# Optimization experiments

Hardware: AMD Instinct MI355X
Metric: run time of the kernel (lower is better)

Reference implementation:

```python
import jax, jax.numpy as jnp
import numpy as np

EPS = 1e-5
NEIGHBOR_K = 3
NEG_SLOPE = 0.2

def _conv(x, w):
    # x: [N,C,H,W], w: [O,I,3,3], stride 1, SAME padding
    return jax.lax.conv_general_dilated(
        x, w, window_strides=(1, 1), padding='SAME',
        dimension_numbers=('NCHW', 'OIHW', 'NCHW'))

def _bn(x, gamma, beta):
    # BatchNorm2d in training mode: batch statistics over (N,H,W), biased var
    m = x.mean(axis=(0, 2, 3), keepdims=True)
    v = x.var(axis=(0, 2, 3), keepdims=True)
    xn = (x - m) * jax.lax.rsqrt(v + EPS)
    return xn * gamma.reshape(1, -1, 1, 1) + beta.reshape(1, -1, 1, 1)

def _lrelu(x):
    return jnp.where(x >= 0, x, NEG_SLOPE * x)

def _maxpool2(x):
    return jax.lax.reduce_window(x, -jnp.inf, jax.lax.max,
                                 (1, 1, 2, 2), (1, 1, 2, 2), 'VALID')

def _features(x, w1, g1, b1, w2, g2, b2, w3, g3, b3, w4, g4, b4):
    x = _maxpool2(_lrelu(_bn(_conv(x, w1), g1, b1)))
    x = _maxpool2(_lrelu(_bn(_conv(x, w2), g2, b2)))
    x = _lrelu(_bn(_conv(x, w3), g3, b3))
    x = _lrelu(_bn(_conv(x, w4), g4, b4))
    return x  # [N, 64, 21, 21]

def setup_inputs() -> dict:
    key = jax.random.key(0)
    ks = jax.random.split(key, 8)
    inp = {
        'input1': jax.random.normal(ks[0], (32, 3, 84, 84), jnp.float32),
        'input2': jax.random.normal(ks[1], (5, 5, 3, 84, 84), jnp.float32),
        'w1': jax.random.normal(ks[2], (64, 3, 3, 3), jnp.float32) * 0.1,
        'g1': jax.random.uniform(ks[3], (64,), jnp.float32, 0.5, 1.5),
        'b1': jnp.zeros((64,), jnp.float32),
        'w2': jax.random.normal(ks[4], (64, 64, 3, 3), jnp.float32) * 0.1,
        'g2': jax.random.uniform(ks[5], (64,), jnp.float32, 0.5, 1.5),
        'b2': jnp.zeros((64,), jnp.float32),
        'w3': jax.random.normal(ks[6], (64, 64, 3, 3), jnp.float32) * 0.1,
        'g3': jax.random.uniform(ks[7], (64,), jnp.float32, 0.5, 1.5),
        'b3': jnp.zeros((64,), jnp.float32),
        'w4': jax.random.normal(jax.random.fold_in(key, 100), (64, 64, 3, 3), jnp.float32) * 0.1,
        'g4': jax.random.uniform(jax.random.fold_in(key, 101), (64,), jnp.float32, 0.5, 1.5),
        'b4': jnp.zeros((64,), jnp.float32),
    }
    return inp

def reference(input1, input2, w1, g1, b1, w2, g2, b2, w3, g3, b3, w4, g4, b4):
    params = (w1, g1, b1, w2, g2, b2, w3, g3, b3, w4, g4, b4)
    # Query features: [B, C, h, w]
    q = _features(input1, *params)
    B, C, h, w = q.shape
    hw = h * w
    Q = q.reshape(B, C, hw).transpose(0, 2, 1)            # [B, hw, C]
    qn = jnp.linalg.norm(Q, axis=2, keepdims=True)        # [B, hw, 1]
    # Support features, BN stats per class-batch (matches per-class forward)
    s = jax.vmap(lambda x: _features(x, *params))(input2) # [nc, shot, C, h, w]
    nc, shot = s.shape[0], s.shape[1]
    S = s.transpose(0, 2, 1, 3, 4).reshape(nc, C, shot * hw)  # [nc, C, M]
    sn = jnp.linalg.norm(S, axis=1, keepdims=True)            # [nc, 1, M]
    # Cosine similarities: [B, nc, hw, M]
    sims = jnp.einsum('bqc,ncm->bnqm', Q, S)
    sims = sims / (qn[:, None, :, :] * sn[None, :, :, :])
    topv = jax.lax.top_k(sims, NEIGHBOR_K)[0]              # [B, nc, hw, k]
    return topv.sum(axis=(2, 3))                           # [B, nc]
```

## Files before the change

kernel.cpp:

```cpp
#include <hip/hip_runtime.h>
#include <hip/hip_bf16.h>
#include <stdint.h>

#define NQ 32
#define NCLS 5
#define SHOT 5
#define NIMG 57
#define P1 7056
#define P2 1764
#define P3 441
#define PX 3528
#define MM (SHOT*P3)
#define EPSB 1e-5f
#define SLOPE 0.2f
#define NEGINF -3.4e38f
#define NREP 32
#define MSPAN 1152
#define MRNG 2
#define QBLK 128
#define NQB 4
#define QG 2
#define SLS 72
#define BNPIX 32

typedef __attribute__((ext_vector_type(8))) short short8;
typedef __attribute__((ext_vector_type(4))) float f32x4;

__device__ __forceinline__ unsigned short bf16bits(float v)
{
    __hip_bfloat16 h = __float2bfloat16(v);
    return *reinterpret_cast<unsigned short*>(&h);
}
__device__ __forceinline__ float bits2f(unsigned short u)
{
    unsigned int x = ((unsigned int)u) << 16;
    return *reinterpret_cast<float*>(&x);
}

__global__ void pack_all_k(const float* __restrict__ w1, const float* __restrict__ w2,
                           const float* __restrict__ w3, const float* __restrict__ w4,
                           unsigned short* __restrict__ wpk1, unsigned short* __restrict__ wpk2,
                           unsigned short* __restrict__ wpk3, unsigned short* __restrict__ wpk4,
                           float* __restrict__ sums)
{
    int i = blockIdx.x * 256 + threadIdx.x;
    if (i < 4 * 6 * 64 * 2 * NREP) sums[i] = 0.f;
    if (i < 3 * 36864) {
        int set = i / 36864, ii = i - set * 36864;
        const float* w = (set == 0) ? w2 : (set == 1) ? w3 : w4;
        unsigned short* wpk = (set == 0) ? wpk2 : (set == 1) ? wpk3 : wpk4;
        int j = ii & 7, lane = (ii >> 3) & 63, chunk = ii >> 9;
        int nt = chunk & 3, half = (chunk >> 2) & 1, t = chunk >> 3;
        int co = nt * 16 + (lane & 15);
        int ci = half * 32 + (lane >> 4) * 8 + j;
        wpk[ii] = bf16bits(w[co * 576 + ci * 9 + t]);
    } else {
        int ii = i - 3 * 36864;
        if (ii >= 4096) return;
        int j = ii & 7, lane = (ii >> 3) & 63, c8 = ii >> 9;
        int nt = c8 & 3, f = c8 >> 2;
        int co = nt * 16 + (lane & 15), q = lane >> 4;
        int k = q * 8 + j;
        float val = 0.f;
        if (f == 0) {
            int t = k >> 2, ci = k & 3;
            if (ci < 3) val = w1[co * 27 + ci * 9 + t];
        } else if (k < 4) {
            int ci = k & 3;
            if (ci < 3) val = w1[co * 27 + ci * 9 + 8];
        }
        wpk1[ii] = bf16bits(val);
    }
}

__global__ __launch_bounds__(256) void conv1m_k(const float* __restrict__ in1,
                                                const float* __restrict__ in2,
                                                const unsigned short* __restrict__ wpk1,
                                                __hip_bfloat16* __restrict__ xpool,
                                                float* __restrict__ sums)
{
    constexpr int S = 84, P = P1, MBLK = 256, NB = 28, SPAN = MBLK + 2 * S + 2;
    __shared__ __align__(16) unsigned short ls4[SPAN * 4];
    __shared__ float qs[4][64], qs2[4][64];
    int img = blockIdx.x / NB;
    int p0 = (blockIdx.x % NB) * MBLK;
    int tid = threadIdx.x, lane = tid & 63, wv = tid >> 6;
    int col = lane & 15, quad = lane >> 4;
    const float* in = (img < NQ) ? in1 + (size_t)img * 3 * P1
                                 : in2 + (size_t)(img - NQ) * 3 * P1;
    for (int u = tid; u < SPAN; u += 256) {
        int p = p0 - S - 1 + u;
        union { unsigned short us[4]; uint2 u2; } o;
        o.u2 = (uint2){0u, 0u};
        if (p >= 0 && p < P) {
            o.us[0] = bf16bits(in[p]);
            o.us[1] = bf16bits(in[P1 + p]);
            o.us[2] = bf16bits(in[2 * P1 + p]);
        }
        *(uint2*)(ls4 + u * 4) = o.u2;
    }
    const short8* wb = (const short8*)wpk1;
    short8 b0[4], b1[4];
    #pragma unroll
    for (int nt = 0; nt < 4; ++nt) {
        b0[nt] = wb[(size_t)(nt * 64 + lane)];
        b1[nt] = wb[(size_t)((4 + nt) * 64 + lane)];
    }
    int t0 = 2 * quad, t1 = t0 + 1;
    int d0 = (t0 / 3 - 1) * S + (t0 % 3 - 1);
    int d1 = (t1 / 3 - 1) * S + (t1 % 3 - 1);
    const int d8 = S + 1;
    int tx0 = t0 % 3, tx1 = t1 % 3;
    __syncthreads();
    f32x4 acc[4][4];
    #pragma unroll
    for (int mt = 0; mt < 4; ++mt)
        #pragma unroll
        for (int nt = 0; nt < 4; ++nt) acc[mt][nt] = (f32x4){0.f, 0.f, 0.f, 0.f};
    #pragma unroll
    for (int mt = 0; mt < 4; ++mt) {
        int pl = wv * 64 + mt * 16 + col;
        int xm = (p0 + pl) % S;
        int base = pl + S + 1;
        uint2 h0 = *(const uint2*)(ls4 + (base + d0) * 4);
        uint2 h1 = *(const uint2*)(ls4 + (base + d1) * 4);
        uint2 h8 = *(const uint2*)(ls4 + (base + d8) * 4);
        bool ok0 = (tx0 == 0) ? (xm >= 1) : ((tx0 == 2) ? (xm <= S - 2) : true);
        bool ok1 = (tx1 == 0) ? (xm >= 1) : ((tx1 == 2) ? (xm <= S - 2) : true);
        bool ok8 = (quad == 0) && (xm <= S - 2);
        if (!ok0) h0 = (uint2){0u, 0u};
        if (!ok1) h1 = (uint2){0u, 0u};
        if (!ok8) h8 = (uint2){0u, 0u};
        union { uint4 u; short8 s; } ca, cb;
        ca.u = (uint4){h0.x, h0.y, h1.x, h1.y};
        cb.u = (uint4){h8.x, h8.y, 0u, 0u};
        #pragma unroll
        for (int nt = 0; nt < 4; ++nt) {
            acc[mt][nt] = __builtin_amdgcn_mfma_f32_16x16x32_bf16(ca.s, b0[nt], acc[mt][nt], 0, 0, 0);
            acc[mt][nt] = __builtin_amdgcn_mfma_f32_16x16x32_bf16(cb.s, b1[nt], acc[mt][nt], 0, 0, 0);
        }
    }
    float s[4] = {0.f, 0.f, 0.f, 0.f}, s2[4] = {0.f, 0.f, 0.f, 0.f};
    __hip_bfloat16* ob = xpool + (size_t)img * PX * 64;
    #pragma unroll
    for (int mt = 0; mt < 4; ++mt) {
        int tb = p0 + wv * 64 + mt * 16 + quad * 4;
        #pragma unroll
        for (int reg = 0; reg < 4; ++reg) {
            int pr = tb + reg;
            if (pr < P) {
                #pragma unroll
                for (int nt = 0; nt < 4; ++nt) {
                    float v = acc[mt][nt][reg];
                    s[nt] += v;
                    s2[nt] = fmaf(v, v, s2[nt]);
                }
            }
        }
        #pragma unroll
        for (int pr2 = 0; pr2 < 2; ++pr2) {
            int m0 = tb + pr2 * 2;
            if (m0 < P) {
                #pragma unroll
                for (int nt = 0; nt < 4; ++nt) {
                    float v = fmaxf(acc[mt][nt][pr2 * 2], acc[mt][nt][pr2 * 2 + 1]);
                    ob[(size_t)(m0 >> 1) * 64 + nt * 16 + col] = __float2bfloat16(v);
                }
            }
        }
    }
    #pragma unroll
    for (int d = 16; d < 64; d <<= 1)
        #pragma unroll
        for (int nt = 0; nt < 4; ++nt) {
            s[nt] += __shfl_xor(s[nt], d, 64);
            s2[nt] += __shfl_xor(s2[nt], d, 64);
        }
    if (quad == 0) {
        #pragma unroll
        for (int nt = 0; nt < 4; ++nt) {
            qs[wv][nt * 16 + col] = s[nt];
            qs2[wv][nt * 16 + col] = s2[nt];
        }
    }
    __syncthreads();
    if (wv == 0) {
        int g = (img < NQ) ? 0 : 1 + (img - NQ) / SHOT;
        int rep = blockIdx.x & (NREP - 1);
        float ts = qs[0][lane] + qs[1][lane] + qs[2][lane] + qs[3][lane];
        float ts2 = qs2[0][lane] + qs2[1][lane] + qs2[2][lane] + qs2[3][lane];
        float* base = sums + ((size_t)(g * 64 + lane) * 2) * NREP + rep;
        atomicAdd(base, ts);
        atomicAdd(base + NREP, ts2);
    }
}

template <int PREVP>
__device__ __forceinline__ void bn_fold(const float* __restrict__ sums_prev,
                                        const float* __restrict__ gamma,
                                        const float* __restrict__ beta,
                                        int g, int tid, float* msl)
{
    if (tid < 64) {
        const float* ps = sums_prev + (size_t)(g * 64 + tid) * 2 * NREP;
        float s = 0.f, s2 = 0.f;
        #pragma unroll
        for (int r = 0; r < NREP; ++r) { s += ps[r]; s2 += ps[NREP + r]; }
        float cnt = (float)((g == 0 ? NQ : SHOT) * PREVP);
        float mean = s / cnt;
        float var = s2 / cnt - mean * mean;
        float a = rsqrtf(var + EPSB) * gamma[tid];
        msl[tid * 2] = a;
        msl[tid * 2 + 1] = fmaf(-mean, a, beta[tid]);
    }
}

template <int S, int MBLK, int MODE, bool POOLX, int PREVP>
__global__ __launch_bounds__(256) void conv64m_k(const unsigned short* __restrict__ inv,
                                                 const unsigned short* __restrict__ wpk,
                                                 __hip_bfloat16* __restrict__ out,
                                                 float* __restrict__ sums,
                                                 const float* __restrict__ sums_prev,
                                                 const float* __restrict__ gamma,
                                                 const float* __restrict__ beta)
{
    constexpr int P = S * S;
    constexpr int MT = MBLK / 64;
    constexpr int NB = (P + MBLK - 1) / MBLK;
    constexpr int SPAN = MBLK + 2 * S + 2;
    __shared__ __align__(16) unsigned short ls[SPAN * 72];
    __shared__ float qs[4][64], qs2[4][64];
    __shared__ float msl[128];
    int img = blockIdx.x / NB;
    int p0 = (blockIdx.x % NB) * MBLK;
    int tid = threadIdx.x;
    int lane = tid & 63, wv = tid >> 6;
    int col = lane & 15, quad = lane >> 4;
    int g = (img < NQ) ? 0 : 1 + (img - NQ) / SHOT;
    bn_fold<PREVP>(sums_prev, gamma, beta, g, tid, msl);
    __syncthreads();
    {
        int part = tid & 7;
        float ba[8], bb[8];
        #pragma unroll
        for (int j = 0; j < 8; ++j) {
            ba[j] = msl[(part * 8 + j) * 2];
            bb[j] = msl[(part * 8 + j) * 2 + 1];
        }
        if constexpr (MODE == 1) {
            const unsigned short* ib = inv + (size_t)img * P * 64;
            for (int u = tid; u < SPAN * 8; u += 256) {
                int pix = u >> 3;
                int p = p0 - S - 1 + pix;
                union { unsigned short us[8]; short8 s8; } o;
                #pragma unroll
                for (int j = 0; j < 8; ++j) o.us[j] = 0;
                if (p >= 0 && p < P) {
                    union { short8 s8; unsigned short us[8]; } x;
                    x.s8 = *(const short8*)(ib + (size_t)p * 64 + part * 8);
                    #pragma unroll
                    for (int j = 0; j < 8; ++j) {
                        float v = fmaf(bits2f(x.us[j]), ba[j], bb[j]);
                        v = fmaxf(v, SLOPE * v);
                        o.us[j] = bf16bits(v);
                    }
                }
                *(short8*)(ls + pix * 72 + part * 8) = o.s8;
            }
        } else {
            const unsigned short* ib2 = inv + (size_t)img * (2 * (size_t)P) * 64;
            for (int u = tid; u < SPAN * 8; u += 256) {
                int pix = u >> 3;
                int p = p0 - S - 1 + pix;
                union { unsigned short us[8]; short8 s8; } o;
                #pragma unroll
                for (int j = 0; j < 8; ++j) o.us[j] = 0;
                if (p >= 0 && p < P) {
                    int y = p / S, x = p - y * S;
                    const unsigned short* src = ib2 + ((size_t)(2 * y) * S + x) * 64 + part * 8;
                    union { short8 s8; unsigned short us[8]; } x0, x1;
                    x0.s8 = *(const short8*)src;
                    x1.s8 = *(const short8*)(src + (size_t)S * 64);
                    #pragma unroll
                    for (int j = 0; j < 8; ++j) {
                        float v = fmaxf(bits2f(x0.us[j]), bits2f(x1.us[j]));
                        v = fmaf(v, ba[j], bb[j]);
                        v = fmaxf(v, SLOPE * v);
                        o.us[j] = bf16bits(v);
                    }
                }
                *(short8*)(ls + pix * 72 + part * 8) = o.s8;
            }
        }
    }
    __syncthreads();
    f32x4 acc[MT][4];
    #pragma unroll
    for (int mt = 0; mt < MT; ++mt)
        #pragma unroll
        for (int nt = 0; nt < 4; ++nt) acc[mt][nt] = (f32x4){0.f, 0.f, 0.f, 0.f};
    bool mok0[MT], mok2[MT];
    #pragma unroll
    for (int mt = 0; mt < MT; ++mt) {
        int xm = (p0 + wv * (MT * 16) + mt * 16 + col) % S;
        mok0[mt] = xm >= 1;
        mok2[mt] = xm <= S - 2;
    }
    const short8* wb = (const short8*)wpk;
    #pragma unroll
    for (int ky = 0; ky < 3; ++ky) {
        #pragma unroll
        for (int kx = 0; kx < 3; ++kx) {
            int t = ky * 3 + kx;
            int d = (ky - 1) * S + (kx - 1);
            #pragma unroll
            for (int half = 0; half < 2; ++half) {
                short8 b[4];
                #pragma unroll
                for (int nt = 0; nt < 4; ++nt)
                    b[nt] = wb[((t * 2 + half) * 4 + nt) * 64 + lane];
                #pragma unroll
                for (int mt = 0; mt < MT; ++mt) {
                    int idx = wv * (MT * 16) + mt * 16 + col + S + 1 + d;
                    short8 a = *(const short8*)(ls + idx * 72 + half * 32 + quad * 8);
                    bool ok = (kx == 0) ? mok0[mt] : (kx == 2) ? mok2[mt] : true;
                    if (!ok) a = (short8){0, 0, 0, 0, 0, 0, 0, 0};
                    #pragma unroll
                    for (int nt = 0; nt < 4; ++nt)
                        acc[mt][nt] = __builtin_amdgcn_mfma_f32_16x16x32_bf16(a, b[nt], acc[mt][nt], 0, 0, 0);
                }
            }
        }
    }
    float s[4] = {0.f, 0.f, 0.f, 0.f}, s2[4] = {0.f, 0.f, 0.f, 0.f};
    __hip_bfloat16* ob = out + (size_t)img * (POOLX ? P / 2 : P) * 64;
    #pragma unroll
    for (int mt = 0; mt < MT; ++mt) {
        int tb = p0 + wv * (MT * 16) + mt * 16 + quad * 4;
        #pragma unroll
        for (int reg = 0; reg < 4; ++reg) {
            int pr = tb + reg;
            if (pr < P) {
                #pragma unroll
                for (int nt = 0; nt < 4; ++nt) {
                    float v = acc[mt][nt][reg];
                    s[nt] += v;
                    s2[nt] = fmaf(v, v, s2[nt]);
                }
            }
        }
        if constexpr (POOLX) {
            #pragma unroll
            for (int pr2 = 0; pr2 < 2; ++pr2) {
                int m0 = tb + pr2 * 2;
                if (m0 < P) {
                    #pragma unroll
                    for (int nt = 0; nt < 4; ++nt) {
                        float v = fmaxf(acc[mt][nt][pr2 * 2], acc[mt][nt][pr2 * 2 + 1]);
                        ob[(size_t)(m0 >> 1) * 64 + nt * 16 + col] = __float2bfloat16(v);
                    }
                }
            }
        } else {
            #pragma unroll
            for (int reg = 0; reg < 4; ++reg) {
                int pr = tb + reg;
                if (pr < P) {
                    #pragma unroll
                    for (int nt = 0; nt < 4; ++nt)
                        ob[(size_t)pr * 64 + nt * 16 + col] = __float2bfloat16(acc[mt][nt][reg]);
                }
            }
        }
    }
    #pragma unroll
    for (int d = 16; d < 64; d <<= 1)
        #pragma unroll
        for (int nt = 0; nt < 4; ++nt) {
            s[nt] += __shfl_xor(s[nt], d, 64);
            s2[nt] += __shfl_xor(s2[nt], d, 64);
        }
    if (quad == 0) {
        #pragma unroll
        for (int nt = 0; nt < 4; ++nt) {
            qs[wv][nt * 16 + col] = s[nt];
            qs2[wv][nt * 16 + col] = s2[nt];
        }
    }
    __syncthreads();
    if (wv == 0) {
        int rep = blockIdx.x & (NREP - 1);
        float ts = qs[0][lane] + qs[1][lane] + qs[2][lane] + qs[3][lane];
        float ts2 = qs2[0][lane] + qs2[1][lane] + qs2[2][lane] + qs2[3][lane];
        float* base = sums + ((size_t)(g * 64 + lane) * 2) * NREP + rep;
        atomicAdd(base, ts);
        atomicAdd(base + NREP, ts2);
    }
}

__global__ __launch_bounds__(256) void bnnorm_k(const unsigned short* __restrict__ x,
                                                const float* __restrict__ sums_prev,
                                                const float* __restrict__ g4,
                                                const float* __restrict__ b4,
                                                __hip_bfloat16* __restrict__ out)
{
    __shared__ float msl[2][128];
    int tid = threadIdx.x;
    int pix0 = blockIdx.x * BNPIX;
    int imgA = pix0 / P3;
    int plast = pix0 + BNPIX - 1; if (plast >= NIMG * P3) plast = NIMG * P3 - 1;
    int imgB = plast / P3;
    int ga = (imgA < NQ) ? 0 : 1 + (imgA - NQ) / SHOT;
    int gb = (imgB < NQ) ? 0 : 1 + (imgB - NQ) / SHOT;
    bn_fold<P3>(sums_prev, g4, b4, ga, tid, msl[0]);
    if (gb != ga) bn_fold<P3>(sums_prev, g4, b4, gb, tid, msl[1]);
    __syncthreads();
    int lane = tid & 63, wvr = tid >> 6;
    int pbase = pix0 + wvr * 8;
    float v[8];
    #pragma unroll
    for (int i = 0; i < 8; ++i) {
        int pix = pbase + i;
        v[i] = (pix < NIMG * P3) ? bits2f(x[(size_t)pix * 64 + lane]) : 0.f;
    }
    #pragma unroll
    for (int i = 0; i < 8; ++i) {
        int pix = pbase + i;
        if (pix >= NIMG * P3) break;
        int img = pix / P3;
        int g = (img < NQ) ? 0 : 1 + (img - NQ) / SHOT;
        const float* ms = msl[(g == ga) ? 0 : 1];
        float w = fmaf(v[i], ms[lane * 2], ms[lane * 2 + 1]);
        w = w >= 0.f ? w : SLOPE * w;
        float ss = w * w;
        #pragma unroll
        for (int d = 32; d > 0; d >>= 1) ss += __shfl_xor(ss, d, 64);
        out[(size_t)pix * 64 + lane] = __float2bfloat16(w * rsqrtf(ss));
    }
}

__device__ __forceinline__ void ins3(float v, float& t0, float& t1, float& t2)
{
    t2 = __builtin_amdgcn_fmed3f(v, t1, t2);
    t1 = __builtin_amdgcn_fmed3f(v, t0, t1);
    t0 = fmaxf(t0, v);
}

template <int PAT>
__device__ __forceinline__ void swzmerge(float& t0, float& t1, float& t2)
{
    float u0 = __int_as_float(__builtin_amdgcn_ds_swizzle(__float_as_int(t0), PAT));
    float u1 = __int_as_float(__builtin_amdgcn_ds_swizzle(__float_as_int(t1), PAT));
    float u2 = __int_as_float(__builtin_amdgcn_ds_swizzle(__float_as_int(t2), PAT));
    ins3(u0, t0, t1, t2);
    ins3(u1, t0, t1, t2);
    ins3(u2, t0, t1, t2);
}

__global__ __launch_bounds__(256) void sim_part_k(const __hip_bfloat16* __restrict__ fhat,
                                                  float* __restrict__ part)
{
    __shared__ __align__(16) unsigned short sl[2][64 * SLS];
    int t = blockIdx.x;
    int mr = t & 1;
    int qb = (t >> 1) & 3;
    int n = (t >> 3) % NCLS;
    int bq = t / (8 * NCLS);
    int tid = threadIdx.x, lane = tid & 63, wv = tid >> 6;
    int col = lane & 15, quad = lane >> 4;
    short8 a0[QG], a1[QG];
    #pragma unroll
    for (int g = 0; g < QG; ++g) {
        int q = qb * QBLK + wv * (QG * 16) + g * 16 + col;
        int qc = q < P3 ? q : P3 - 1;
        const unsigned short* qp = (const unsigned short*)fhat + ((size_t)bq * P3 + qc) * 64;
        a0[g] = *(const short8*)(qp + quad * 8);
        a1[g] = *(const short8*)(qp + 32 + quad * 8);
    }
    const unsigned short* sp = (const unsigned short*)fhat + (size_t)(NQ + n * SHOT) * P3 * 64;
    int m_lo = mr * MSPAN;
    int m_cnt = MM - m_lo; if (m_cnt > MSPAN) m_cnt = MSPAN;
    int nfull = m_cnt >> 6;
    int rem = m_cnt & 63;
    float t0[QG][4], t1[QG][4], t2[QG][4];
    #pragma unroll
    for (int g = 0; g < QG; ++g)
        #pragma unroll
        for (int r = 0; r < 4; ++r) { t0[g][r] = NEGINF; t1[g][r] = NEGINF; t2[g][r] = NEGINF; }
    int srow = tid >> 3, scc = (tid & 7) * 8;
    const unsigned short* gp = sp + (size_t)(m_lo + srow) * 64 + scc;
    unsigned short* ld0 = &sl[0][srow * SLS + scc];
    unsigned short* ld1 = &sl[1][srow * SLS + scc];
    const short8 z8 = {0, 0, 0, 0, 0, 0, 0, 0};
    short8 v0 = *(const short8*)gp;
    short8 v1 = *(const short8*)(gp + 32 * 64);
    *(short8*)ld0 = v0;
    *(short8*)(ld0 + 32 * SLS) = v1;
    __syncthreads();
    int cur = 0;
    for (int c = 0; c < nfull; ++c) {
        bool nf = (c + 1 < nfull);
        bool np = (c + 1 == nfull) && (rem != 0);
        if (nf) {
            gp += 64 * 64;
            v0 = *(const short8*)gp;
            v1 = *(const short8*)(gp + 32 * 64);
        } else if (np) {
            gp += 64 * 64;
            v0 = (srow < rem) ? *(const short8*)gp : z8;
            v1 = z8;
        }
        const unsigned short* sr = &sl[cur][col * SLS + quad * 8];
        #pragma unroll
        for (int mt = 0; mt < 4; ++mt) {
            short8 b0 = *(const short8*)(sr + mt * (16 * SLS));
            short8 b1 = *(const short8*)(sr + mt * (16 * SLS) + 32);
            #pragma unroll
            for (int g = 0; g < QG; ++g) {
                f32x4 acc = {0.f, 0.f, 0.f, 0.f};
                acc = __builtin_amdgcn_mfma_f32_16x16x32_bf16(a0[g], b0, acc, 0, 0, 0);
                acc = __builtin_amdgcn_mfma_f32_16x16x32_bf16(a1[g], b1, acc, 0, 0, 0);
                #pragma unroll
                for (int r = 0; r < 4; ++r) ins3(acc[r], t0[g][r], t1[g][r], t2[g][r]);
            }
        }
        if (nf | np) {
            unsigned short* ld = (cur == 0) ? ld1 : ld0;
            *(short8*)ld = v0;
            *(short8*)(ld + 32 * SLS) = v1;
        }
        __syncthreads();
        cur ^= 1;
    }
    if (rem) {
        const unsigned short* sr = &sl[cur][col * SLS + quad * 8];
        int ptiles = (rem + 15) >> 4;
        for (int mt = 0; mt < ptiles; ++mt) {
            short8 b0 = *(const short8*)(sr + mt * (16 * SLS));
            short8 b1 = *(const short8*)(sr + mt * (16 * SLS) + 32);
            bool valid = (mt * 16 + col) < rem;
            #pragma unroll
            for (int g = 0; g < QG; ++g) {
                f32x4 acc = {0.f, 0.f, 0.f, 0.f};
                acc = __builtin_amdgcn_mfma_f32_16x16x32_bf16(a0[g], b0, acc, 0, 0, 0);
                acc = __builtin_amdgcn_mfma_f32_16x16x32_bf16(a1[g], b1, acc, 0, 0, 0);
                #pragma unroll
                for (int r = 0; r < 4; ++r)
                    ins3(valid ? acc[r] : NEGINF, t0[g][r], t1[g][r], t2[g][r]);
            }
        }
    }
    #pragma unroll
    for (int g = 0; g < QG; ++g)
        #pragma unroll
        for (int r = 0; r < 4; ++r) {
            swzmerge<0x041F>(t0[g][r], t1[g][r], t2[g][r]);
            swzmerge<0x081F>(t0[g][r], t1[g][r], t2[g][r]);
            swzmerge<0x101F>(t0[g][r], t1[g][r], t2[g][r]);
            swzmerge<0x201F>(t0[g][r], t1[g][r], t2[g][r]);
        }
    if (col == 0) {
        #pragma unroll
        for (int g = 0; g < QG; ++g)
            #pragma unroll
            for (int r = 0; r < 4; ++r) {
                int ql = wv * (QG * 16) + g * 16 + quad * 4 + r;
                float* pp = part + ((((size_t)(bq * NCLS + n) * NQB + qb) * MRNG + mr) * QBLK + ql) * 3;
                pp[0] = t0[g][r];
                pp[1] = t1[g][r];
                pp[2] = t2[g][r];
            }
    }
}

__global__ __launch_bounds__(256) void sim_merge_k(const float* __restrict__ part,
                                                   float* __restrict__ out)
{
    __shared__ float red[4];
    int b = blockIdx.x;
    int tid = threadIdx.x, lane = tid & 63, wv = tid >> 6;
    float s = 0.f;
    for (int q = tid; q < P3; q += 256) {
        int qb = q >> 7, ql = q & 127;
        const float* pp = part + (((size_t)b * NQB + qb) * MRNG * QBLK + ql) * 3;
        float v0 = pp[0], v1 = pp[1], v2 = pp[2];
        #pragma unroll
        for (int mr = 1; mr < MRNG; ++mr) {
            const float* pm = pp + (size_t)mr * (QBLK * 3);
            ins3(pm[0], v0, v1, v2);
            ins3(pm[1], v0, v1, v2);
            ins3(pm[2], v0, v1, v2);
        }
        s += v0 + v1 + v2;
    }
    #pragma unroll
    for (int d = 32; d > 0; d >>= 1) s += __shfl_xor(s, d, 64);
    if (lane == 0) red[wv] = s;
    __syncthreads();
    if (tid == 0) out[b] = red[0] + red[1] + red[2] + red[3];
}

extern "C" void kernel_launch(void* const* d_in, const int* in_sizes, int n_in,
                              void* d_out, int out_size, void* d_ws, size_t ws_size,
                              hipStream_t stream)
{
    const float* input1 = (const float*)d_in[0];
    const float* input2 = (const float*)d_in[1];
    const float* w1 = (const float*)d_in[2];
    const float* g1 = (const float*)d_in[3];
    const float* b1 = (const float*)d_in[4];
    const float* w2 = (const float*)d_in[5];
    const float* g2 = (const float*)d_in[6];
    const float* b2 = (const float*)d_in[7];
    const float* w3 = (const float*)d_in[8];
    const float* g3 = (const float*)d_in[9];
    const float* b3 = (const float*)d_in[10];
    const float* w4 = (const float*)d_in[11];
    const float* g4 = (const float*)d_in[12];
    const float* b4 = (const float*)d_in[13];
    float* out = (float*)d_out;

    char* w8 = (char*)d_ws;
    const size_t oB = 51480576;
    const size_t oT = oB + 12870144;
    const size_t STG = 6 * 64 * 2 * NREP * sizeof(float);
    __hip_bfloat16* xpool1 = (__hip_bfloat16*)(w8 + 0);
    __hip_bfloat16* conv3raw = (__hip_bfloat16*)(w8 + 0);
    __hip_bfloat16* conv4raw = (__hip_bfloat16*)(w8 + 9652608);
    __hip_bfloat16* fhat = (__hip_bfloat16*)(w8 + 16087680);
    __hip_bfloat16* xpool2 = (__hip_bfloat16*)(w8 + oB);
    float* sums = (float*)(w8 + oT);
    unsigned short* wpk2 = (unsigned short*)(w8 + oT + 4 * STG + 12288);
    unsigned short* wpk3 = (unsigned short*)(w8 + oT + 4 * STG + 12288 + 73728);
    unsigned short* wpk4 = (unsigned short*)(w8 + oT + 4 * STG + 12288 + 147456);
    unsigned short* wpk1 = (unsigned short*)(w8 + oT + 4 * STG + 12288 + 221184);
    const size_t oP = oT + 4 * STG + 12288 + 221184 + 8192;
    float* part = (float*)(w8 + oP);
    if (ws_size < oP + (size_t)NQ * NCLS * NQB * MRNG * QBLK * 3 * sizeof(float)) return;
    float* sums1 = sums;
    float* sums2 = sums + 6 * 64 * 2 * NREP;
    float* sums3 = sums2 + 6 * 64 * 2 * NREP;
    float* sums4 = sums3 + 6 * 64 * 2 * NREP;

    pack_all_k<<<448, 256, 0, stream>>>(w1, w2, w3, w4, wpk1, wpk2, wpk3, wpk4, sums);

    conv1m_k<<<NIMG * 28, 256, 0, stream>>>(input1, input2, wpk1, xpool1, sums1);
    conv64m_k<42, 128, 2, true, P1><<<NIMG * 14, 256, 0, stream>>>(
        (const unsigned short*)xpool1, wpk2, xpool2, sums2, sums1, g1, b1);
    conv64m_k<21, 64, 2, false, P2><<<NIMG * 7, 256, 0, stream>>>(
        (const unsigned short*)xpool2, wpk3, conv3raw, sums3, sums2, g2, b2);
    conv64m_k<21, 64, 1, false, P3><<<NIMG * 7, 256, 0, stream>>>(
        (const unsigned short*)conv3raw, wpk4, conv4raw, sums4, sums3, g3, b3);
    bnnorm_k<<<(NIMG * P3 + BNPIX - 1) / BNPIX, 256, 0, stream>>>(
        (const unsigned short*)conv4raw, sums4, g4, b4, fhat);
    sim_part_k<<<NQ * NCLS * NQB * MRNG, 256, 0, stream>>>(fhat, part);
    sim_merge_k<<<NQ * NCLS, 256, 0, stream>>>(part, out);
}
```

Before: 212.2 us.

## Fuse full 2x2 maxpool into conv1 by processing two image rows per block

Each conv1 block now covers two full 84-pixel rows instead of 256 arbitrary pixels. The horizontal pair maxima are staged in shared memory, and the vertical max is taken before writing a 42x42 pooled bf16 output. The conv2 stage is told its input is already fully pooled, which roughly halves the intermediate buffer it writes and reads. The cost is more blocks, each doing less MFMA work and carrying extra shared-memory staging, plus an added barrier.

Measured after the change: 217.7 us. +2.6%, slower.

```diff
diff --git a/kernel.cpp b/kernel.cpp
--- a/kernel.cpp
+++ b/kernel.cpp
@@ -9,7 +9,6 @@
 #define P1 7056
 #define P2 1764
 #define P3 441
-#define PX 3528
 #define MM (SHOT*P3)
 #define EPSB 1e-5f
 #define SLOPE 0.2f
@@ -79,11 +78,13 @@
                                                 __hip_bfloat16* __restrict__ xpool,
                                                 float* __restrict__ sums)
 {
-    constexpr int S = 84, P = P1, MBLK = 256, NB = 28, SPAN = MBLK + 2 * S + 2;
-    __shared__ __align__(16) unsigned short ls4[SPAN * 4];
+    constexpr int S = 84, P = P1, MB = 168, SPAN = MB + 2 * S + 2;
+    __shared__ __align__(16) unsigned short ls4[384 * 4];
+    __shared__ float xmx[2 * 42 * 64];
     __shared__ float qs[4][64], qs2[4][64];
-    int img = blockIdx.x / NB;
-    int p0 = (blockIdx.x % NB) * MBLK;
+    int img = blockIdx.x / 42;
+    int rp = blockIdx.x % 42;
+    int p0 = rp * MB;
     int tid = threadIdx.x, lane = tid & 63, wv = tid >> 6;
     int col = lane & 15, quad = lane >> 4;
     const float* in = (img < NQ) ? in1 + (size_t)img * 3 * P1
@@ -112,15 +113,15 @@
     const int d8 = S + 1;
     int tx0 = t0 % 3, tx1 = t1 % 3;
     __syncthreads();
-    f32x4 acc[4][4];
-    #pragma unroll
-    for (int mt = 0; mt < 4; ++mt)
+    f32x4 acc[3][4];
+    #pragma unroll
+    for (int mt = 0; mt < 3; ++mt)
         #pragma unroll
         for (int nt = 0; nt < 4; ++nt) acc[mt][nt] = (f32x4){0.f, 0.f, 0.f, 0.f};
     #pragma unroll
-    for (int mt = 0; mt < 4; ++mt) {
-        int pl = wv * 64 + mt * 16 + col;
-        int xm = (p0 + pl) % S;
+    for (int mt = 0; mt < 3; ++mt) {
+        int pl = wv * 48 + mt * 16 + col;
+        int xm = pl % S;
         int base = pl + S + 1;
         uint2 h0 = *(const uint2*)(ls4 + (base + d0) * 4);
         uint2 h1 = *(const uint2*)(ls4 + (base + d1) * 4);
@@ -141,14 +142,13 @@
         }
     }
     float s[4] = {0.f, 0.f, 0.f, 0.f}, s2[4] = {0.f, 0.f, 0.f, 0.f};
-    __hip_bfloat16* ob = xpool + (size_t)img * PX * 64;
-    #pragma unroll
-    for (int mt = 0; mt < 4; ++mt) {
-        int tb = p0 + wv * 64 + mt * 16 + quad * 4;
+    #pragma unroll
+    for (int mt = 0; mt < 3; ++mt) {
+        int tb = wv * 48 + mt * 16 + quad * 4;
         #pragma unroll
         for (int reg = 0; reg < 4; ++reg) {
             int pr = tb + reg;
-            if (pr < P) {
+            if (pr < MB) {
                 #pragma unroll
                 for (int nt = 0; nt < 4; ++nt) {
                     float v = acc[mt][nt][reg];
@@ -160,14 +160,23 @@
         #pragma unroll
         for (int pr2 = 0; pr2 < 2; ++pr2) {
             int m0 = tb + pr2 * 2;
-            if (m0 < P) {
+            if (m0 < MB) {
+                int r = (m0 >= S) ? 1 : 0;
+                int xo = (m0 - r * S) >> 1;
                 #pragma unroll
                 for (int nt = 0; nt < 4; ++nt) {
                     float v = fmaxf(acc[mt][nt][pr2 * 2], acc[mt][nt][pr2 * 2 + 1]);
-                    ob[(size_t)(m0 >> 1) * 64 + nt * 16 + col] = __float2bfloat16(v);
-                }
-            }
-        }
+                    xmx[(r * 42 + xo) * 64 + nt * 16 + col] = v;
+                }
+            }
+        }
+    }
+    __syncthreads();
+    __hip_bfloat16* ob = xpool + (size_t)img * P2 * 64;
+    for (int i = tid; i < 42 * 64; i += 256) {
+        int xo = i >> 6, ch = i & 63;
+        float v = fmaxf(xmx[xo * 64 + ch], xmx[(42 + xo) * 64 + ch]);
+        ob[((size_t)(rp * 42 + xo)) * 64 + ch] = __float2bfloat16(v);
     }
     #pragma unroll
     for (int d = 16; d < 64; d <<= 1)
@@ -644,8 +653,8 @@
 
     pack_all_k<<<448, 256, 0, stream>>>(w1, w2, w3, w4, wpk1, wpk2, wpk3, wpk4, sums);
 
-    conv1m_k<<<NIMG * 28, 256, 0, stream>>>(input1, input2, wpk1, xpool1, sums1);
-    conv64m_k<42, 128, 2, true, P1><<<NIMG * 14, 256, 0, stream>>>(
+    conv1m_k<<<NIMG * 42, 256, 0, stream>>>(input1, input2, wpk1, xpool1, sums1);
+    conv64m_k<42, 128, 1, true, P1><<<NIMG * 14, 256, 0, stream>>>(
         (const unsigned short*)xpool1, wpk2, xpool2, sums2, sums1, g1, b1);
     conv64m_k<21, 64, 2, false, P2><<<NIMG * 7, 256, 0, stream>>>(
         (const unsigned short*)xpool2, wpk3, conv3raw, sums3, sums2, g2, b2);
```
